# Kernel tuning notes

Measured on AMD Instinct MI355X. Metric: run time of the kernel, lower is better.

Reference implementation:

```python
import jax, jax.numpy as jnp
import numpy as np

N = 50000        # N_particles
E = 800000       # edges (avg degree 16)
SD = 32          # state_dim = 3 + 2*2 + 25
OC = 16          # message_out_channels
H = 32           # MLP hidden_channels
BN_EPS = 1e-5


def _bn(h, g, b):
    # PyG MLP default BatchNorm1d, training-mode batch stats over rows
    m = h.mean(axis=0)
    v = h.var(axis=0)
    return (h - m) * jax.lax.rsqrt(v + BN_EPS) * g + b


def _mlp3(h, w1, b1, g1, be1, w2, b2, g2, be2, w3, b3):
    # Linear -> BN -> ReLU, Linear -> BN -> ReLU, Linear
    h = jax.nn.relu(_bn(h @ w1 + b1, g1, be1))
    h = jax.nn.relu(_bn(h @ w2 + b2, g2, be2))
    return h @ w3 + b3


def setup_inputs() -> dict:
    key = jax.random.key(0)
    ks = jax.random.split(key, 16)

    def rn(k, shape):
        fan_in = shape[0] if len(shape) > 1 else shape[0]
        return jax.random.normal(k, shape, jnp.float32) / np.sqrt(fan_in)

    inp = {
        "x": jax.random.normal(ks[0], (N, SD), jnp.float32),
        "edge_attr": jax.random.normal(ks[1], (E, SD), jnp.float32),
        "edge_index": jax.random.randint(ks[2], (2, E), 0, N, jnp.int64),
        # edge-weight-generating MLP: SD -> 32 -> 32 -> SD*OC
        "msg_w1": rn(ks[3], (SD, H)), "msg_b1": jnp.zeros((H,), jnp.float32),
        "msg_g1": jnp.ones((H,), jnp.float32), "msg_be1": jnp.zeros((H,), jnp.float32),
        "msg_w2": rn(ks[4], (H, H)), "msg_b2": jnp.zeros((H,), jnp.float32),
        "msg_g2": jnp.ones((H,), jnp.float32), "msg_be2": jnp.zeros((H,), jnp.float32),
        "msg_w3": rn(ks[5], (H, SD * OC)), "msg_b3": jnp.zeros((SD * OC,), jnp.float32),
        # NNConv root weight + bias
        "root_w": rn(ks[6], (SD, OC)), "root_b": jnp.zeros((OC,), jnp.float32),
        # own_state_nn MLP: (SD+OC) -> 32 -> 32 -> SD
        "own_w1": rn(ks[7], (SD + OC, H)), "own_b1": jnp.zeros((H,), jnp.float32),
        "own_g1": jnp.ones((H,), jnp.float32), "own_be1": jnp.zeros((H,), jnp.float32),
        "own_w2": rn(ks[8], (H, H)), "own_b2": jnp.zeros((H,), jnp.float32),
        "own_g2": jnp.ones((H,), jnp.float32), "own_be2": jnp.zeros((H,), jnp.float32),
        "own_w3": rn(ks[9], (H, SD)), "own_b3": jnp.zeros((SD,), jnp.float32),
    }
    return inp


def reference(x, edge_attr, edge_index,
              msg_w1, msg_b1, msg_g1, msg_be1, msg_w2, msg_b2, msg_g2, msg_be2,
              msg_w3, msg_b3, root_w, root_b,
              own_w1, own_b1, own_g1, own_be1, own_w2, own_b2, own_g2, own_be2,
              own_w3, own_b3):
    src, dst = edge_index[0], edge_index[1]
    # per-edge weight matrices: [E, SD, OC]
    W_e = _mlp3(edge_attr, msg_w1, msg_b1, msg_g1, msg_be1,
                msg_w2, msg_b2, msg_g2, msg_be2, msg_w3, msg_b3)
    W_e = W_e.reshape(-1, SD, OC)
    # gather-matmul-scatter (NNConv, aggr='add')
    msg = jnp.einsum('ei,eio->eo', x[src], W_e)          # [E, OC]
    agg = jax.ops.segment_sum(msg, dst, num_segments=N)  # [N, OC]
    messages = agg + x @ root_w + root_b                 # root weight + bias
    combined = jnp.concatenate([x, messages], axis=-1)   # [N, SD+OC]
    new_state = _mlp3(combined, own_w1, own_b1, own_g1, own_be1,
                      own_w2, own_b2, own_g2, own_be2, own_w3, own_b3)
    return new_state
```

## Files before the change

### kernel.cpp

```cpp
#include <hip/hip_runtime.h>
#include <hip/hip_fp16.h>


#define N_NODES 50000
#define N_EDGES 800000
#define SD 32
#define OC 16
#define HID 32
#define BN_EPS 1e-5f
#define ETILES 3125
#define NTILES 196

#define OFF_STATS 0u
#define OFF_DEGS  1024u
#define OFF_CURS  201024u
#define OFF_DEGD  401024u
#define OFF_CURD  601024u
#define OFF_BASES 801024u
#define OFF_BASED 1001088u
#define OFF_PERM  1201152u
#define OFF_POSD  4401152u
#define OFF_XB    7601152u
#define OFF_AGG   10801152u
#define OFF_H2S   14001152u
#define OFF_MSGB  65201152u

__device__ __forceinline__ float f4get(const float4& v, int ii) {
  return ii == 0 ? v.x : ii == 1 ? v.y : ii == 2 ? v.z : v.w;
}

__device__ __forceinline__ unsigned pack2(float a, float b) {
  __half2 h = __floats2half2_rn(a, b);
  return *reinterpret_cast<unsigned*>(&h);
}
__device__ __forceinline__ void unpk8(uint4 u, float* o) {
  __half2 a = *reinterpret_cast<__half2*>(&u.x), b = *reinterpret_cast<__half2*>(&u.y);
  __half2 c = *reinterpret_cast<__half2*>(&u.z), d = *reinterpret_cast<__half2*>(&u.w);
  float2 fa = __half22float2(a), fb = __half22float2(b);
  float2 fc = __half22float2(c), fd = __half22float2(d);
  o[0] = fa.x; o[1] = fa.y; o[2] = fb.x; o[3] = fb.y;
  o[4] = fc.x; o[5] = fc.y; o[6] = fd.x; o[7] = fd.y;
}

template<int I4, int IOFF>
__device__ __forceinline__ void mv_acc(const float4* __restrict__ rp,
                                       const float* __restrict__ wlds,
                                       float z[HID]) {
#pragma unroll
  for (int i4 = 0; i4 < I4; ++i4) {
    float4 rv = rp[i4];
#pragma unroll
    for (int ii = 0; ii < 4; ++ii) {
      float s = f4get(rv, ii);
      const float* wrow = wlds + (IOFF + i4 * 4 + ii) * HID;
#pragma unroll
      for (int h4 = 0; h4 < HID / 4; ++h4) {
        float4 wv = *reinterpret_cast<const float4*>(wrow + h4 * 4);
        z[h4 * 4 + 0] = fmaf(s, wv.x, z[h4 * 4 + 0]);
        z[h4 * 4 + 1] = fmaf(s, wv.y, z[h4 * 4 + 1]);
        z[h4 * 4 + 2] = fmaf(s, wv.z, z[h4 * 4 + 2]);
        z[h4 * 4 + 3] = fmaf(s, wv.w, z[h4 * 4 + 3]);
      }
    }
  }
}

__device__ __forceinline__ void mv_reg(const float* __restrict__ v,
                                       const float* __restrict__ wlds,
                                       float z[HID]) {
#pragma unroll
  for (int h = 0; h < HID; ++h) z[h] = 0.f;
#pragma unroll
  for (int i = 0; i < HID; ++i) {
    float s = v[i];
    const float* wrow = wlds + i * HID;
#pragma unroll
    for (int h4 = 0; h4 < HID / 4; ++h4) {
      float4 wv = *reinterpret_cast<const float4*>(wrow + h4 * 4);
      z[h4 * 4 + 0] = fmaf(s, wv.x, z[h4 * 4 + 0]);
      z[h4 * 4 + 1] = fmaf(s, wv.y, z[h4 * 4 + 1]);
      z[h4 * 4 + 2] = fmaf(s, wv.z, z[h4 * 4 + 2]);
      z[h4 * 4 + 3] = fmaf(s, wv.w, z[h4 * 4 + 3]);
    }
  }
}

__device__ __forceinline__ void bn_params(const float* __restrict__ stats, int off,
                                          float cntInv, const float* __restrict__ g,
                                          const float* __restrict__ be,
                                          float* __restrict__ sc, float* __restrict__ sf) {
  if (threadIdx.x < HID) {
    int h = threadIdx.x;
    float mean = stats[off + h] * cntInv;
    float var = stats[off + HID + h] * cntInv - mean * mean;
    float s = g[h] * rsqrtf(var + BN_EPS);
    sc[h] = s;
    sf[h] = fmaf(-mean, s, be[h]);
  }
}

__device__ __forceinline__ void tile_accum(const float z[HID], float* __restrict__ tile,
                                           int h, int g, float& s, float& q) {
  int tid = threadIdx.x;
  __syncthreads();
#pragma unroll
  for (int j = 0; j < HID; ++j) tile[tid * 33 + j] = z[j];
  __syncthreads();
#pragma unroll
  for (int k = 0; k < 32; ++k) {
    float v = tile[(g * 32 + k) * 33 + h];
    s += v;
    q = fmaf(v, v, q);
  }
}

__device__ __forceinline__ void tile_finish(float* __restrict__ tile, int h, int g,
                                            float s, float q,
                                            float* __restrict__ gstats) {
  int tid = threadIdx.x;
  __syncthreads();
  tile[g * 32 + h] = s;
  tile[256 + g * 32 + h] = q;
  __syncthreads();
  if (tid < 64) {
    int hh = tid & 31;
    int base = (tid < 32) ? 0 : 256;
    float acc = 0.f;
#pragma unroll
    for (int g2 = 0; g2 < 8; ++g2) acc += tile[base + g2 * 32 + hh];
    atomicAdd(gstats + ((tid < 32) ? hh : (HID + hh)), acc);
  }
}

__global__ __launch_bounds__(256) void kH(const int* __restrict__ ei,
                                          int* __restrict__ degS, int* __restrict__ degD) {
  int e = blockIdx.x * 256 + threadIdx.x;
  atomicAdd(degS + ei[e], 1);
  atomicAdd(degD + ei[N_EDGES + e], 1);
}

__global__ __launch_bounds__(1024) void kScan(const int* __restrict__ degS, int* __restrict__ baseS,
                                              const int* __restrict__ degD, int* __restrict__ baseD) {
  __shared__ int sc[1024];
  const int* deg = (blockIdx.x == 0) ? degS : degD;
  int* base = (blockIdx.x == 0) ? baseS : baseD;
  int t = threadIdx.x;
  const int C = 49;
  int st = t * C;
  int sum = 0;
  for (int k = 0; k < C; ++k) {
    int i = st + k;
    if (i < N_NODES) sum += deg[i];
  }
  sc[t] = sum;
  __syncthreads();
  for (int s = 1; s < 1024; s <<= 1) {
    int v = (t >= s) ? sc[t - s] : 0;
    __syncthreads();
    sc[t] += v;
    __syncthreads();
  }
  int run = sc[t] - sum;
  for (int k = 0; k < C; ++k) {
    int i = st + k;
    if (i < N_NODES) { base[i] = run; run += deg[i]; }
  }
  if (t == 1023) base[N_NODES] = run;
}

__global__ __launch_bounds__(256) void kRank(const int* __restrict__ ei,
    const int* __restrict__ baseS, const int* __restrict__ baseD,
    int* __restrict__ curS, int* __restrict__ curD,
    int* __restrict__ perm, int* __restrict__ posD) {
  int e = blockIdx.x * 256 + threadIdx.x;
  int s = ei[e], d = ei[N_EDGES + e];
  int rs = atomicAdd(curS + s, 1);
  perm[baseS[s] + rs] = e;
  int rd = atomicAdd(curD + d, 1);
  posD[e] = baseD[d] + rd;
}

__global__ __launch_bounds__(256) void k0_nodes(
    const float* __restrict__ x, const float* __restrict__ b3,
    const float* __restrict__ rootw, const float* __restrict__ rootb,
    float* __restrict__ xb, float* __restrict__ agg) {
  __shared__ float xs[16][33];
  int n0 = blockIdx.x * 16;
  for (int f = threadIdx.x; f < 16 * SD; f += 256) {
    int nl = f >> 5, i = f & 31;
    xs[nl][i] = x[(size_t)(n0 + nl) * SD + i];
  }
  __syncthreads();
  int nl = threadIdx.x >> 4, o = threadIdx.x & 15;
  int n = n0 + nl;
  float a1 = 0.f, a2 = 0.f;
#pragma unroll
  for (int i = 0; i < SD; ++i) {
    float xv = xs[nl][i];
    a1 = fmaf(xv, b3[i * OC + o], a1);
    a2 = fmaf(xv, rootw[i * OC + o], a2);
  }
  xb[(size_t)n * OC + o] = a1;
  agg[(size_t)n * OC + o] = a2 + rootb[o];
}

__global__ __launch_bounds__(256) void s1_edge(
    const float* __restrict__ ea, const float* __restrict__ w1,
    float* __restrict__ stats) {
  __shared__ float w1s[SD * HID];
  __shared__ float tile[256 * 33];
  for (int f = threadIdx.x; f < SD * HID; f += 256) w1s[f] = w1[f];
  int h = threadIdx.x & 31, g = threadIdx.x >> 5;
  float s = 0.f, q = 0.f;
  __syncthreads();
#pragma unroll 1
  for (int t = blockIdx.x; t < ETILES; t += gridDim.x) {
    int e = t * 256 + threadIdx.x;
    const float4* rp = reinterpret_cast<const float4*>(ea + (size_t)e * SD);
    float z[HID];
#pragma unroll
    for (int j = 0; j < HID; ++j) z[j] = 0.f;
    mv_acc<8, 0>(rp, w1s, z);
    tile_accum(z, tile, h, g, s, q);
  }
  tile_finish(tile, h, g, s, q, stats + 0);
}

__global__ __launch_bounds__(256) void s2_edge(
    const float* __restrict__ ea, const float* __restrict__ w1,
    const float* __restrict__ w2, const float* __restrict__ g1,
    const float* __restrict__ be1, float* __restrict__ stats,
    __half* __restrict__ h2s) {
  __shared__ float w1s[SD * HID], w2s[HID * HID];
  __shared__ float sc1[HID], sf1[HID];
  __shared__ float tile[256 * 33];
  for (int f = threadIdx.x; f < SD * HID; f += 256) w1s[f] = w1[f];
  for (int f = threadIdx.x; f < HID * HID; f += 256) w2s[f] = w2[f];
  bn_params(stats, 0, 1.f / N_EDGES, g1, be1, sc1, sf1);
  int h = threadIdx.x & 31, g = threadIdx.x >> 5;
  float s = 0.f, q = 0.f;
  __syncthreads();
#pragma unroll 1
  for (int t = blockIdx.x; t < ETILES; t += gridDim.x) {
    int e = t * 256 + threadIdx.x;
    const float4* rp = reinterpret_cast<const float4*>(ea + (size_t)e * SD);
    float z1[HID];
#pragma unroll
    for (int j = 0; j < HID; ++j) z1[j] = 0.f;
    mv_acc<8, 0>(rp, w1s, z1);
#pragma unroll
    for (int i = 0; i < HID; ++i) z1[i] = fmaxf(0.f, fmaf(z1[i], sc1[i], sf1[i]));
    float z2[HID];
    mv_reg(z1, w2s, z2);
    unsigned us[16];
#pragma unroll
    for (int q2 = 0; q2 < 16; ++q2) us[q2] = pack2(z2[2 * q2], z2[2 * q2 + 1]);
    uint4* hp = reinterpret_cast<uint4*>(h2s + (size_t)e * HID);
    hp[0] = make_uint4(us[0], us[1], us[2], us[3]);
    hp[1] = make_uint4(us[4], us[5], us[6], us[7]);
    hp[2] = make_uint4(us[8], us[9], us[10], us[11]);
    hp[3] = make_uint4(us[12], us[13], us[14], us[15]);
    tile_accum(z2, tile, h, g, s, q);
  }
  tile_finish(tile, h, g, s, q, stats + 64);
}

__global__ __launch_bounds__(256) void k5_gemm(
    const float* __restrict__ x, const float* __restrict__ w3,
    const int* __restrict__ perm, const int* __restrict__ posD,
    const int* __restrict__ baseS, const float* __restrict__ xb,
    const __half* __restrict__ h2s, const float* __restrict__ stats,
    const float* __restrict__ g2, const float* __restrict__ be2,
    __half* __restrict__ msgb) {
  __shared__ float Tl[16 * 516];
  __shared__ float xsl[16][33];
  __shared__ float xbl[256];
  __shared__ int bSl[17];
  __shared__ float sc2[HID], sf2[HID];
  int tid = threadIdx.x;
  int n0 = blockIdx.x * 16;
  for (int f = tid; f < 16 * SD; f += 256)
    xsl[f >> 5][f & 31] = x[(size_t)(n0 + (f >> 5)) * SD + (f & 31)];
  xbl[tid] = xb[(size_t)n0 * OC + tid];
  if (tid < 17) bSl[tid] = baseS[n0 + tid];
  bn_params(stats, 64, 1.f / N_EDGES, g2, be2, sc2, sf2);
  __syncthreads();
  {
    int oH = tid & 1, h = (tid >> 1) & 31, ng = tid >> 6;
    float acc[4][8];
#pragma unroll
    for (int k = 0; k < 4; ++k)
#pragma unroll
      for (int j = 0; j < 8; ++j) acc[k][j] = 0.f;
    const float* wbase = w3 + h * (SD * OC) + oH * 8;
#pragma unroll
    for (int i = 0; i < SD; ++i) {
      float4 wa = *reinterpret_cast<const float4*>(wbase + i * OC);
      float4 wb = *reinterpret_cast<const float4*>(wbase + i * OC + 4);
#pragma unroll
      for (int k = 0; k < 4; ++k) {
        float xv = xsl[ng * 4 + k][i];
        acc[k][0] = fmaf(xv, wa.x, acc[k][0]);
        acc[k][1] = fmaf(xv, wa.y, acc[k][1]);
        acc[k][2] = fmaf(xv, wa.z, acc[k][2]);
        acc[k][3] = fmaf(xv, wa.w, acc[k][3]);
        acc[k][4] = fmaf(xv, wb.x, acc[k][4]);
        acc[k][5] = fmaf(xv, wb.y, acc[k][5]);
        acc[k][6] = fmaf(xv, wb.z, acc[k][6]);
        acc[k][7] = fmaf(xv, wb.w, acc[k][7]);
      }
    }
#pragma unroll
    for (int k = 0; k < 4; ++k)
#pragma unroll
      for (int jj = 0; jj < 8; ++jj)
        Tl[(ng * 4 + k) * 516 + (oH * 8 + jj) * 32 + h] = acc[k][jj];
  }
  __syncthreads();
  int jbeg = bSl[0], jend = bSl[16];
  for (int j = jbeg + tid; j < jend; j += 256) {
    int nl = 0;
    while (j >= bSl[nl + 1]) ++nl;
    int e = perm[j];
    float h2v[HID];
    const uint4* hp = reinterpret_cast<const uint4*>(h2s + (size_t)e * HID);
    uint4 u0 = hp[0], u1 = hp[1], u2 = hp[2], u3 = hp[3];
    unpk8(u0, h2v + 0); unpk8(u1, h2v + 8);
    unpk8(u2, h2v + 16); unpk8(u3, h2v + 24);
#pragma unroll
    for (int k = 0; k < HID; ++k) h2v[k] = fmaxf(0.f, fmaf(h2v[k], sc2[k], sf2[k]));
    float m[OC];
#pragma unroll
    for (int o = 0; o < OC; ++o) m[o] = xbl[nl * 16 + o];
#pragma unroll
    for (int o = 0; o < OC; ++o) {
      const float* tb = Tl + nl * 516 + o * 32;
      float a = m[o];
#pragma unroll
      for (int h4 = 0; h4 < 8; ++h4) {
        float4 t = *reinterpret_cast<const float4*>(tb + h4 * 4);
        a = fmaf(h2v[h4 * 4 + 0], t.x, a);
        a = fmaf(h2v[h4 * 4 + 1], t.y, a);
        a = fmaf(h2v[h4 * 4 + 2], t.z, a);
        a = fmaf(h2v[h4 * 4 + 3], t.w, a);
      }
      m[o] = a;
    }
    int dp = posD[e];
    unsigned us[8];
#pragma unroll
    for (int q = 0; q < 8; ++q) us[q] = pack2(m[2 * q], m[2 * q + 1]);
    uint4* mp = reinterpret_cast<uint4*>(msgb + (size_t)dp * OC);
    mp[0] = make_uint4(us[0], us[1], us[2], us[3]);
    mp[1] = make_uint4(us[4], us[5], us[6], us[7]);
  }
}

__global__ __launch_bounds__(256) void k5_aggr(
    const int* __restrict__ baseD, const __half* __restrict__ msgb,
    float* __restrict__ agg) {
  int tid = threadIdx.x;
  int d = blockIdx.x * 16 + (tid >> 4);
  int o = tid & 15;
  int b0 = baseD[d], b1 = baseD[d + 1];
  float s = 0.f;
  for (int j = b0; j < b1; ++j) s += __half2float(msgb[(size_t)j * OC + o]);
  agg[(size_t)d * OC + o] += s;
}

__global__ __launch_bounds__(256) void s1_own(
    const float* __restrict__ x, const float* __restrict__ msgs,
    const float* __restrict__ w1, float* __restrict__ stats) {
  __shared__ float w1s[(SD + OC) * HID];
  __shared__ float tile[256 * 33];
  for (int f = threadIdx.x; f < (SD + OC) * HID; f += 256) w1s[f] = w1[f];
  int h = threadIdx.x & 31, g = threadIdx.x >> 5;
  float s = 0.f, q = 0.f;
  __syncthreads();
#pragma unroll 1
  for (int t = blockIdx.x; t < NTILES; t += gridDim.x) {
    int n = t * 256 + threadIdx.x;
    float z[HID];
#pragma unroll
    for (int j = 0; j < HID; ++j) z[j] = 0.f;
    if (n < N_NODES) {
      const float4* xp = reinterpret_cast<const float4*>(x + (size_t)n * SD);
      const float4* mp = reinterpret_cast<const float4*>(msgs + (size_t)n * OC);
      mv_acc<8, 0>(xp, w1s, z);
      mv_acc<4, SD>(mp, w1s, z);
    }
    tile_accum(z, tile, h, g, s, q);
  }
  tile_finish(tile, h, g, s, q, stats + 128);
}

__global__ __launch_bounds__(256) void s2_own(
    const float* __restrict__ x, const float* __restrict__ msgs,
    const float* __restrict__ w1, const float* __restrict__ w2,
    const float* __restrict__ g1, const float* __restrict__ be1,
    float* __restrict__ stats) {
  __shared__ float w1s[(SD + OC) * HID], w2s[HID * HID];
  __shared__ float sc1[HID], sf1[HID];
  __shared__ float tile[256 * 33];
  for (int f = threadIdx.x; f < (SD + OC) * HID; f += 256) w1s[f] = w1[f];
  for (int f = threadIdx.x; f < HID * HID; f += 256) w2s[f] = w2[f];
  bn_params(stats, 128, 1.f / N_NODES, g1, be1, sc1, sf1);
  int h = threadIdx.x & 31, g = threadIdx.x >> 5;
  float s = 0.f, q = 0.f;
  __syncthreads();
#pragma unroll 1
  for (int t = blockIdx.x; t < NTILES; t += gridDim.x) {
    int n = t * 256 + threadIdx.x;
    float z2[HID];
#pragma unroll
    for (int j = 0; j < HID; ++j) z2[j] = 0.f;
    if (n < N_NODES) {
      const float4* xp = reinterpret_cast<const float4*>(x + (size_t)n * SD);
      const float4* mp = reinterpret_cast<const float4*>(msgs + (size_t)n * OC);
      float z1[HID];
#pragma unroll
      for (int j = 0; j < HID; ++j) z1[j] = 0.f;
      mv_acc<8, 0>(xp, w1s, z1);
      mv_acc<4, SD>(mp, w1s, z1);
#pragma unroll
      for (int i = 0; i < HID; ++i) z1[i] = fmaxf(0.f, fmaf(z1[i], sc1[i], sf1[i]));
      mv_reg(z1, w2s, z2);
    }
    tile_accum(z2, tile, h, g, s, q);
  }
  tile_finish(tile, h, g, s, q, stats + 192);
}

__global__ __launch_bounds__(256) void k10_own_out(
    const float* __restrict__ x, const float* __restrict__ msgs,
    const float* __restrict__ w1, const float* __restrict__ w2,
    const float* __restrict__ w3o, const float* __restrict__ b3o,
    const float* __restrict__ g1, const float* __restrict__ be1,
    const float* __restrict__ g2, const float* __restrict__ be2,
    const float* __restrict__ stats, float* __restrict__ out) {
  __shared__ float w1s[(SD + OC) * HID], w2s[HID * HID], w3s[HID * SD];
  __shared__ float sc1[HID], sf1[HID], sc2[HID], sf2[HID];
  for (int f = threadIdx.x; f < (SD + OC) * HID; f += 256) w1s[f] = w1[f];
  for (int f = threadIdx.x; f < HID * HID; f += 256) w2s[f] = w2[f];
  for (int f = threadIdx.x; f < HID * SD; f += 256) w3s[f] = w3o[f];
  bn_params(stats, 128, 1.f / N_NODES, g1, be1, sc1, sf1);
  bn_params(stats, 192, 1.f / N_NODES, g2, be2, sc2, sf2);
  __syncthreads();
  int n = blockIdx.x * 256 + threadIdx.x;
  if (n >= N_NODES) return;
  const float4* xp = reinterpret_cast<const float4*>(x + (size_t)n * SD);
  const float4* mp = reinterpret_cast<const float4*>(msgs + (size_t)n * OC);
  float z1[HID];
#pragma unroll
  for (int j = 0; j < HID; ++j) z1[j] = 0.f;
  mv_acc<8, 0>(xp, w1s, z1);
  mv_acc<4, SD>(mp, w1s, z1);
#pragma unroll
  for (int i = 0; i < HID; ++i) z1[i] = fmaxf(0.f, fmaf(z1[i], sc1[i], sf1[i]));
  float z2[HID];
  mv_reg(z1, w2s, z2);
#pragma unroll
  for (int i = 0; i < HID; ++i) z2[i] = fmaxf(0.f, fmaf(z2[i], sc2[i], sf2[i]));
  float z3[HID];
  mv_reg(z2, w3s, z3);
  float4* op = reinterpret_cast<float4*>(out + (size_t)n * SD);
#pragma unroll
  for (int j4 = 0; j4 < 8; ++j4) {
    op[j4] = make_float4(z3[j4 * 4 + 0] + b3o[j4 * 4 + 0],
                         z3[j4 * 4 + 1] + b3o[j4 * 4 + 1],
                         z3[j4 * 4 + 2] + b3o[j4 * 4 + 2],
                         z3[j4 * 4 + 3] + b3o[j4 * 4 + 3]);
  }
}

extern "C" void kernel_launch(void* const* d_in, const int* in_sizes, int n_in,
                              void* d_out, int out_size, void* d_ws, size_t ws_size,
                              hipStream_t stream) {
  const float* x    = (const float*)d_in[0];
  const float* ea   = (const float*)d_in[1];
  const int*   ei   = (const int*)d_in[2];
  const float* mw1  = (const float*)d_in[3];
  const float* mg1  = (const float*)d_in[5];
  const float* mbe1 = (const float*)d_in[6];
  const float* mw2  = (const float*)d_in[7];
  const float* mg2  = (const float*)d_in[9];
  const float* mbe2 = (const float*)d_in[10];
  const float* mw3  = (const float*)d_in[11];
  const float* mb3  = (const float*)d_in[12];
  const float* rw   = (const float*)d_in[13];
  const float* rb   = (const float*)d_in[14];
  const float* ow1  = (const float*)d_in[15];
  const float* og1  = (const float*)d_in[17];
  const float* obe1 = (const float*)d_in[18];
  const float* ow2  = (const float*)d_in[19];
  const float* og2  = (const float*)d_in[21];
  const float* obe2 = (const float*)d_in[22];
  const float* ow3  = (const float*)d_in[23];
  const float* ob3  = (const float*)d_in[24];
  float* out = (float*)d_out;

  char* ws = (char*)d_ws;
  float* stats = (float*)(ws + OFF_STATS);
  int* degS  = (int*)(ws + OFF_DEGS);
  int* curS  = (int*)(ws + OFF_CURS);
  int* degD  = (int*)(ws + OFF_DEGD);
  int* curD  = (int*)(ws + OFF_CURD);
  int* baseS = (int*)(ws + OFF_BASES);
  int* baseD = (int*)(ws + OFF_BASED);
  int* perm  = (int*)(ws + OFF_PERM);
  int* posD  = (int*)(ws + OFF_POSD);
  float* xb  = (float*)(ws + OFF_XB);
  float* agg = (float*)(ws + OFF_AGG);
  __half* h2s  = (__half*)(ws + OFF_H2S);
  __half* msgb = (__half*)(ws + OFF_MSGB);

  hipMemsetAsync(ws, 0, 801024, stream);

  kH<<<3125, 256, 0, stream>>>(ei, degS, degD);
  kScan<<<2, 1024, 0, stream>>>(degS, baseS, degD, baseD);
  kRank<<<3125, 256, 0, stream>>>(ei, baseS, baseD, curS, curD, perm, posD);
  k0_nodes<<<3125, 256, 0, stream>>>(x, mb3, rw, rb, xb, agg);
  s1_edge<<<1024, 256, 0, stream>>>(ea, mw1, stats);
  s2_edge<<<1024, 256, 0, stream>>>(ea, mw1, mw2, mg1, mbe1, stats, h2s);
  k5_gemm<<<3125, 256, 0, stream>>>(x, mw3, perm, posD, baseS, xb, h2s,
                                    stats, mg2, mbe2, msgb);
  k5_aggr<<<3125, 256, 0, stream>>>(baseD, msgb, agg);
  s1_own<<<NTILES, 256, 0, stream>>>(x, agg, ow1, stats);
  s2_own<<<NTILES, 256, 0, stream>>>(x, agg, ow1, ow2, og1, obe1, stats);
  k10_own_out<<<(N_NODES + 255) / 256, 256, 0, stream>>>(
      x, agg, ow1, ow2, ow3, ob3, og1, obe1, og2, obe2, stats, out);
}
```

Before: 739.8 us.

## Compute BN1 stats via Gram matrix, sort h2 by source, fuse aggregation with own-MLP stats

The first edge BatchNorm's statistics are now computed algebraically. A 32x32 Gram matrix and the column sums of edge_attr (sM_edge) are projected through w1 (kBN1), so the per-edge 32-wide matvec pass is no longer needed for them. s2_edge writes h2 in source-sorted order, and kRank emits a packed word holding destination position and local node index. This lets k5_gemm read h2 contiguously without the perm indirection or the linear node search. k0_nodes is folded into k5_gemm and the new aggregation kernel, and s1_own is fused into aggregation with atomic per-block stats. This trades extra atomics and a scattered h2 write for less edge-level compute and indirection.

```diff
diff --git a/kernel.cpp b/kernel.cpp
--- a/kernel.cpp
+++ b/kernel.cpp
@@ -12,18 +12,19 @@
 #define NTILES 196
 
 #define OFF_STATS 0u
-#define OFF_DEGS  1024u
-#define OFF_CURS  201024u
-#define OFF_DEGD  401024u
-#define OFF_CURD  601024u
-#define OFF_BASES 801024u
-#define OFF_BASED 1001088u
-#define OFF_PERM  1201152u
-#define OFF_POSD  4401152u
-#define OFF_XB    7601152u
-#define OFF_AGG   10801152u
-#define OFF_H2S   14001152u
-#define OFF_MSGB  65201152u
+#define OFF_M     1024u
+#define OFF_EASUM 5120u
+#define OFF_DEGS  5376u
+#define OFF_CURS  205376u
+#define OFF_DEGD  405376u
+#define OFF_CURD  605376u
+#define OFF_BASES 805376u
+#define OFF_BASED 1005440u
+#define OFF_POSS  1205504u
+#define OFF_COMBO 4405504u
+#define OFF_AGG   7605504u
+#define OFF_H2S   10805504u
+#define OFF_MSGB  62005504u
 
 __device__ __forceinline__ float f4get(const float4& v, int ii) {
   return ii == 0 ? v.x : ii == 1 ? v.y : ii == 2 ? v.z : v.w;
@@ -171,66 +172,82 @@
 __global__ __launch_bounds__(256) void kRank(const int* __restrict__ ei,
     const int* __restrict__ baseS, const int* __restrict__ baseD,
     int* __restrict__ curS, int* __restrict__ curD,
-    int* __restrict__ perm, int* __restrict__ posD) {
+    int* __restrict__ posS, unsigned* __restrict__ combo) {
   int e = blockIdx.x * 256 + threadIdx.x;
   int s = ei[e], d = ei[N_EDGES + e];
   int rs = atomicAdd(curS + s, 1);
-  perm[baseS[s] + rs] = e;
+  int ps = baseS[s] + rs;
+  posS[e] = ps;
   int rd = atomicAdd(curD + d, 1);
-  posD[e] = baseD[d] + rd;
-}
-
-__global__ __launch_bounds__(256) void k0_nodes(
-    const float* __restrict__ x, const float* __restrict__ b3,
-    const float* __restrict__ rootw, const float* __restrict__ rootb,
-    float* __restrict__ xb, float* __restrict__ agg) {
-  __shared__ float xs[16][33];
-  int n0 = blockIdx.x * 16;
-  for (int f = threadIdx.x; f < 16 * SD; f += 256) {
-    int nl = f >> 5, i = f & 31;
-    xs[nl][i] = x[(size_t)(n0 + nl) * SD + i];
-  }
-  __syncthreads();
-  int nl = threadIdx.x >> 4, o = threadIdx.x & 15;
-  int n = n0 + nl;
-  float a1 = 0.f, a2 = 0.f;
-#pragma unroll
-  for (int i = 0; i < SD; ++i) {
-    float xv = xs[nl][i];
-    a1 = fmaf(xv, b3[i * OC + o], a1);
-    a2 = fmaf(xv, rootw[i * OC + o], a2);
-  }
-  xb[(size_t)n * OC + o] = a1;
-  agg[(size_t)n * OC + o] = a2 + rootb[o];
-}
-
-__global__ __launch_bounds__(256) void s1_edge(
-    const float* __restrict__ ea, const float* __restrict__ w1,
-    float* __restrict__ stats) {
-  __shared__ float w1s[SD * HID];
-  __shared__ float tile[256 * 33];
-  for (int f = threadIdx.x; f < SD * HID; f += 256) w1s[f] = w1[f];
-  int h = threadIdx.x & 31, g = threadIdx.x >> 5;
-  float s = 0.f, q = 0.f;
-  __syncthreads();
+  combo[ps] = (unsigned)(baseD[d] + rd) | ((unsigned)(s & 15) << 27);
+}
+
+__global__ __launch_bounds__(256) void sM_edge(const float* __restrict__ ea,
+                                               float* __restrict__ M,
+                                               float* __restrict__ easum) {
+  __shared__ float t[256 * 36];
+  int tid = threadIdx.x;
+  int i = tid >> 3, j4 = tid & 7;
+  float a0 = 0.f, a1 = 0.f, a2 = 0.f, a3 = 0.f, cs = 0.f;
 #pragma unroll 1
-  for (int t = blockIdx.x; t < ETILES; t += gridDim.x) {
-    int e = t * 256 + threadIdx.x;
-    const float4* rp = reinterpret_cast<const float4*>(ea + (size_t)e * SD);
-    float z[HID];
-#pragma unroll
-    for (int j = 0; j < HID; ++j) z[j] = 0.f;
-    mv_acc<8, 0>(rp, w1s, z);
-    tile_accum(z, tile, h, g, s, q);
-  }
-  tile_finish(tile, h, g, s, q, stats + 0);
+  for (int tb = blockIdx.x; tb < ETILES; tb += gridDim.x) {
+    __syncthreads();
+    const float4* src = reinterpret_cast<const float4*>(ea + (size_t)tb * (256 * SD));
+#pragma unroll
+    for (int u = 0; u < 8; ++u) {
+      int idx = u * 256 + tid;
+      float4 v = src[idx];
+      *reinterpret_cast<float4*>(&t[(idx >> 3) * 36 + (idx & 7) * 4]) = v;
+    }
+    __syncthreads();
+#pragma unroll 4
+    for (int k = 0; k < 256; ++k) {
+      float s = t[k * 36 + i];
+      float4 v = *reinterpret_cast<const float4*>(&t[k * 36 + j4 * 4]);
+      a0 = fmaf(s, v.x, a0); a1 = fmaf(s, v.y, a1);
+      a2 = fmaf(s, v.z, a2); a3 = fmaf(s, v.w, a3);
+      if (j4 == 0) cs += s;
+    }
+  }
+  atomicAdd(M + i * 32 + j4 * 4 + 0, a0);
+  atomicAdd(M + i * 32 + j4 * 4 + 1, a1);
+  atomicAdd(M + i * 32 + j4 * 4 + 2, a2);
+  atomicAdd(M + i * 32 + j4 * 4 + 3, a3);
+  if (j4 == 0) atomicAdd(easum + i, cs);
+}
+
+__global__ __launch_bounds__(1024) void kBN1(const float* __restrict__ M,
+                                             const float* __restrict__ easum,
+                                             const float* __restrict__ w1,
+                                             float* __restrict__ stats) {
+  __shared__ float Ms[1024], w1s[1024], part[32 * 33];
+  int tid = threadIdx.x;
+  Ms[tid] = M[tid];
+  w1s[tid] = w1[tid];
+  __syncthreads();
+  int h = tid & 31, i = tid >> 5;
+  float tacc = 0.f;
+#pragma unroll
+  for (int j = 0; j < 32; ++j) tacc = fmaf(Ms[i * 32 + j], w1s[j * 32 + h], tacc);
+  part[i * 33 + h] = w1s[i * 32 + h] * tacc;
+  __syncthreads();
+  if (tid < 32) {
+    float sq = 0.f, sm = 0.f;
+#pragma unroll
+    for (int i2 = 0; i2 < 32; ++i2) {
+      sq += part[i2 * 33 + tid];
+      sm = fmaf(easum[i2], w1s[i2 * 32 + tid], sm);
+    }
+    stats[tid] = sm;
+    stats[32 + tid] = sq;
+  }
 }
 
 __global__ __launch_bounds__(256) void s2_edge(
-    const float* __restrict__ ea, const float* __restrict__ w1,
-    const float* __restrict__ w2, const float* __restrict__ g1,
-    const float* __restrict__ be1, float* __restrict__ stats,
-    __half* __restrict__ h2s) {
+    const float* __restrict__ ea, const int* __restrict__ posS,
+    const float* __restrict__ w1, const float* __restrict__ w2,
+    const float* __restrict__ g1, const float* __restrict__ be1,
+    float* __restrict__ stats, __half* __restrict__ h2s) {
   __shared__ float w1s[SD * HID], w2s[HID * HID];
   __shared__ float sc1[HID], sf1[HID];
   __shared__ float tile[256 * 33];
@@ -252,10 +269,11 @@
     for (int i = 0; i < HID; ++i) z1[i] = fmaxf(0.f, fmaf(z1[i], sc1[i], sf1[i]));
     float z2[HID];
     mv_reg(z1, w2s, z2);
+    int ps = posS[e];
     unsigned us[16];
 #pragma unroll
     for (int q2 = 0; q2 < 16; ++q2) us[q2] = pack2(z2[2 * q2], z2[2 * q2 + 1]);
-    uint4* hp = reinterpret_cast<uint4*>(h2s + (size_t)e * HID);
+    uint4* hp = reinterpret_cast<uint4*>(h2s + (size_t)ps * HID);
     hp[0] = make_uint4(us[0], us[1], us[2], us[3]);
     hp[1] = make_uint4(us[4], us[5], us[6], us[7]);
     hp[2] = make_uint4(us[8], us[9], us[10], us[11]);
@@ -267,32 +285,40 @@
 
 __global__ __launch_bounds__(256) void k5_gemm(
     const float* __restrict__ x, const float* __restrict__ w3,
-    const int* __restrict__ perm, const int* __restrict__ posD,
-    const int* __restrict__ baseS, const float* __restrict__ xb,
-    const __half* __restrict__ h2s, const float* __restrict__ stats,
-    const float* __restrict__ g2, const float* __restrict__ be2,
-    __half* __restrict__ msgb) {
+    const float* __restrict__ b3, const unsigned* __restrict__ combo,
+    const int* __restrict__ baseS, const __half* __restrict__ h2s,
+    const float* __restrict__ stats, const float* __restrict__ g2,
+    const float* __restrict__ be2, __half* __restrict__ msgb) {
   __shared__ float Tl[16 * 516];
   __shared__ float xsl[16][33];
   __shared__ float xbl[256];
-  __shared__ int bSl[17];
+  __shared__ float b3s[SD * OC];
   __shared__ float sc2[HID], sf2[HID];
+  __shared__ int jr[2];
   int tid = threadIdx.x;
   int n0 = blockIdx.x * 16;
   for (int f = tid; f < 16 * SD; f += 256)
-    xsl[f >> 5][f & 31] = x[(size_t)(n0 + (f >> 5)) * SD + (f & 31)];
-  xbl[tid] = xb[(size_t)n0 * OC + tid];
-  if (tid < 17) bSl[tid] = baseS[n0 + tid];
+    xsl[f >> 5][f & 31] = x[(size_t)n0 * SD + f];
+  for (int f = tid; f < SD * OC; f += 256) b3s[f] = b3[f];
+  if (tid == 0) jr[0] = baseS[n0];
+  if (tid == 1) jr[1] = baseS[n0 + 16];
   bn_params(stats, 64, 1.f / N_EDGES, g2, be2, sc2, sf2);
   __syncthreads();
   {
-    int oH = tid & 1, h = (tid >> 1) & 31, ng = tid >> 6;
+    int nl = tid >> 4, o = tid & 15;
+    float a1 = 0.f;
+#pragma unroll
+    for (int i = 0; i < SD; ++i) a1 = fmaf(xsl[nl][i], b3s[i * OC + o], a1);
+    xbl[tid] = a1;
+  }
+  {
+    int oH = tid & 1, hh = (tid >> 1) & 31, ng = tid >> 6;
     float acc[4][8];
 #pragma unroll
     for (int k = 0; k < 4; ++k)
 #pragma unroll
       for (int j = 0; j < 8; ++j) acc[k][j] = 0.f;
-    const float* wbase = w3 + h * (SD * OC) + oH * 8;
+    const float* wbase = w3 + hh * (SD * OC) + oH * 8;
 #pragma unroll
     for (int i = 0; i < SD; ++i) {
       float4 wa = *reinterpret_cast<const float4*>(wbase + i * OC);
@@ -314,17 +340,17 @@
     for (int k = 0; k < 4; ++k)
 #pragma unroll
       for (int jj = 0; jj < 8; ++jj)
-        Tl[(ng * 4 + k) * 516 + (oH * 8 + jj) * 32 + h] = acc[k][jj];
-  }
-  __syncthreads();
-  int jbeg = bSl[0], jend = bSl[16];
+        Tl[(ng * 4 + k) * 516 + (oH * 8 + jj) * 32 + hh] = acc[k][jj];
+  }
+  __syncthreads();
+  int jbeg = jr[0], jend = jr[1];
   for (int j = jbeg + tid; j < jend; j += 256) {
-    int nl = 0;
-    while (j >= bSl[nl + 1]) ++nl;
-    int e = perm[j];
+    unsigned c = combo[j];
+    int dp = (int)(c & 0x07FFFFFFu);
+    int nl = (int)(c >> 27);
+    const uint4* hp = reinterpret_cast<const uint4*>(h2s + (size_t)j * HID);
+    uint4 u0 = hp[0], u1 = hp[1], u2 = hp[2], u3 = hp[3];
     float h2v[HID];
-    const uint4* hp = reinterpret_cast<const uint4*>(h2s + (size_t)e * HID);
-    uint4 u0 = hp[0], u1 = hp[1], u2 = hp[2], u3 = hp[3];
     unpk8(u0, h2v + 0); unpk8(u1, h2v + 8);
     unpk8(u2, h2v + 16); unpk8(u3, h2v + 24);
 #pragma unroll
@@ -346,7 +372,6 @@
       }
       m[o] = a;
     }
-    int dp = posD[e];
     unsigned us[8];
 #pragma unroll
     for (int q = 0; q < 8; ++q) us[q] = pack2(m[2 * q], m[2 * q + 1]);
@@ -356,42 +381,63 @@
   }
 }
 
-__global__ __launch_bounds__(256) void k5_aggr(
+__global__ __launch_bounds__(256) void k6_aggr_own(
     const int* __restrict__ baseD, const __half* __restrict__ msgb,
-    float* __restrict__ agg) {
+    const float* __restrict__ x, const float* __restrict__ rootw,
+    const float* __restrict__ rootb, const float* __restrict__ ow1,
+    float* __restrict__ agg, float* __restrict__ stats) {
+  __shared__ float xsl[16][33];
+  __shared__ float aggl[16 * 17];
+  __shared__ float rws[SD * OC];
+  __shared__ float ow1s[(SD + OC) * HID];
+  __shared__ float zt[16 * 33];
+  __shared__ float rbs[OC];
   int tid = threadIdx.x;
-  int d = blockIdx.x * 16 + (tid >> 4);
-  int o = tid & 15;
+  int n0 = blockIdx.x * 16;
+  for (int f = tid; f < 16 * SD; f += 256) xsl[f >> 5][f & 31] = x[(size_t)n0 * SD + f];
+  for (int f = tid; f < SD * OC; f += 256) rws[f] = rootw[f];
+  for (int f = tid; f < (SD + OC) * HID; f += 256) ow1s[f] = ow1[f];
+  if (tid < OC) rbs[tid] = rootb[tid];
+  __syncthreads();
+  int nl = tid >> 4, o = tid & 15;
+  int d = n0 + nl;
+  float r = rbs[o];
+#pragma unroll
+  for (int i = 0; i < SD; ++i) r = fmaf(xsl[nl][i], rws[i * OC + o], r);
   int b0 = baseD[d], b1 = baseD[d + 1];
   float s = 0.f;
   for (int j = b0; j < b1; ++j) s += __half2float(msgb[(size_t)j * OC + o]);
-  agg[(size_t)d * OC + o] += s;
-}
-
-__global__ __launch_bounds__(256) void s1_own(
-    const float* __restrict__ x, const float* __restrict__ msgs,
-    const float* __restrict__ w1, float* __restrict__ stats) {
-  __shared__ float w1s[(SD + OC) * HID];
-  __shared__ float tile[256 * 33];
-  for (int f = threadIdx.x; f < (SD + OC) * HID; f += 256) w1s[f] = w1[f];
-  int h = threadIdx.x & 31, g = threadIdx.x >> 5;
-  float s = 0.f, q = 0.f;
-  __syncthreads();
-#pragma unroll 1
-  for (int t = blockIdx.x; t < NTILES; t += gridDim.x) {
-    int n = t * 256 + threadIdx.x;
-    float z[HID];
-#pragma unroll
-    for (int j = 0; j < HID; ++j) z[j] = 0.f;
-    if (n < N_NODES) {
-      const float4* xp = reinterpret_cast<const float4*>(x + (size_t)n * SD);
-      const float4* mp = reinterpret_cast<const float4*>(msgs + (size_t)n * OC);
-      mv_acc<8, 0>(xp, w1s, z);
-      mv_acc<4, SD>(mp, w1s, z);
-    }
-    tile_accum(z, tile, h, g, s, q);
-  }
-  tile_finish(tile, h, g, s, q, stats + 128);
+  float val = r + s;
+  agg[(size_t)d * OC + o] = val;
+  aggl[nl * 17 + o] = val;
+  __syncthreads();
+  float za = 0.f, zb = 0.f;
+#pragma unroll
+  for (int i = 0; i < SD; ++i) {
+    float xv = xsl[nl][i];
+    za = fmaf(xv, ow1s[i * HID + o], za);
+    zb = fmaf(xv, ow1s[i * HID + o + 16], zb);
+  }
+#pragma unroll
+  for (int i = 0; i < OC; ++i) {
+    float mv = aggl[nl * 17 + i];
+    za = fmaf(mv, ow1s[(SD + i) * HID + o], za);
+    zb = fmaf(mv, ow1s[(SD + i) * HID + o + 16], zb);
+  }
+  zt[nl * 33 + o] = za;
+  zt[nl * 33 + o + 16] = zb;
+  __syncthreads();
+  if (tid < 64) {
+    int h = tid & 31;
+    bool issq = tid >= 32;
+    float acc = 0.f;
+#pragma unroll
+    for (int k = 0; k < 16; ++k) {
+      float v = zt[k * 33 + h];
+      acc += issq ? v * v : v;
+    }
+    atomicAdd(stats + 128 + (issq ? 32 : 0) + h, acc);
+  }
 }
 
 __global__ __launch_bounds__(256) void s2_own(
@@ -500,32 +546,32 @@
   float* out = (float*)d_out;
 
   char* ws = (char*)d_ws;
-  float* stats = (float*)(ws + OFF_STATS);
-  int* degS  = (int*)(ws + OFF_DEGS);
-  int* curS  = (int*)(ws + OFF_CURS);
-  int* degD  = (int*)(ws + OFF_DEGD);
-  int* curD  = (int*)(ws + OFF_CURD);
-  int* baseS = (int*)(ws + OFF_BASES);
-  int* baseD = (int*)(ws + OFF_BASED);
-  int* perm  = (int*)(ws + OFF_PERM);
-  int* posD  = (int*)(ws + OFF_POSD);
-  float* xb  = (float*)(ws + OFF_XB);
-  float* agg = (float*)(ws + OFF_AGG);
-  __half* h2s  = (__half*)(ws + OFF_H2S);
-  __half* msgb = (__half*)(ws + OFF_MSGB);
-
-  hipMemsetAsync(ws, 0, 801024, stream);
+  float* stats  = (float*)(ws + OFF_STATS);
+  float* M      = (float*)(ws + OFF_M);
+  float* easum  = (float*)(ws + OFF_EASUM);
+  int* degS     = (int*)(ws + OFF_DEGS);
+  int* curS     = (int*)(ws + OFF_CURS);
+  int* degD     = (int*)(ws + OFF_DEGD);
+  int* curD     = (int*)(ws + OFF_CURD);
+  int* baseS    = (int*)(ws + OFF_BASES);
+  int* baseD    = (int*)(ws + OFF_BASED);
+  int* posS     = (int*)(ws + OFF_POSS);
+  unsigned* combo = (unsigned*)(ws + OFF_COMBO);
+  float* agg    = (float*)(ws + OFF_AGG);
+  __half* h2s   = (__half*)(ws + OFF_H2S);
+  __half* msgb  = (__half*)(ws + OFF_MSGB);
+
+  hipMemsetAsync(ws, 0, 805376, stream);
 
   kH<<<3125, 256, 0, stream>>>(ei, degS, degD);
   kScan<<<2, 1024, 0, stream>>>(degS, baseS, degD, baseD);
-  kRank<<<3125, 256, 0, stream>>>(ei, baseS, baseD, curS, curD, perm, posD);
-  k0_nodes<<<3125, 256, 0, stream>>>(x, mb3, rw, rb, xb, agg);
-  s1_edge<<<1024, 256, 0, stream>>>(ea, mw1, stats);
-  s2_edge<<<1024, 256, 0, stream>>>(ea, mw1, mw2, mg1, mbe1, stats, h2s);
-  k5_gemm<<<3125, 256, 0, stream>>>(x, mw3, perm, posD, baseS, xb, h2s,
+  kRank<<<3125, 256, 0, stream>>>(ei, baseS, baseD, curS, curD, posS, combo);
+  sM_edge<<<1024, 256, 0, stream>>>(ea, M, easum);
+  kBN1<<<1, 1024, 0, stream>>>(M, easum, mw1, stats);
+  s2_edge<<<1024, 256, 0, stream>>>(ea, posS, mw1, mw2, mg1, mbe1, stats, h2s);
+  k5_gemm<<<3125, 256, 0, stream>>>(x, mw3, mb3, combo, baseS, h2s,
                                     stats, mg2, mbe2, msgb);
-  k5_aggr<<<3125, 256, 0, stream>>>(baseD, msgb, agg);
-  s1_own<<<NTILES, 256, 0, stream>>>(x, agg, ow1, stats);
+  k6_aggr_own<<<3125, 256, 0, stream>>>(baseD, msgb, x, rw, rb, ow1, agg, stats);
   s2_own<<<NTILES, 256, 0, stream>>>(x, agg, ow1, ow2, og1, obe1, stats);
   k10_own_out<<<(N_NODES + 255) / 256, 256, 0, stream>>>(
       x, agg, ow1, ow2, ow3, ob3, og1, obe1, og2, obe2, stats, out);
```

Measured after the change: 853.9 us. +15.4%, slower.
